# Kernel tuning notes

Hardware: AMD Instinct MI355X
Metric: run time of the kernel (lower is better)

Reference implementation:

```python
import jax, jax.numpy as jnp
import numpy as np

BETA = 20.0  # Softplus beta in the original torch module
# upper-triangular (offset=1) indices of a 3x3 matrix, matching torch.triu_indices(3,3,1)
TRIU_R = np.array([0, 0, 1])
TRIU_C = np.array([1, 2, 2])


def _softplus(x):
    # torch.nn.Softplus(beta=20): log(1+exp(beta*x))/beta, numerically stable via jax.nn.softplus
    return jax.nn.softplus(BETA * x) / BETA


def setup_inputs() -> dict:
    key = jax.random.key(0)
    ks = jax.random.split(key, 9)
    N = 1_000_000
    h = 32

    def lin_init(k, fan_in, fan_out):
        bound = 1.0 / np.sqrt(fan_in)
        kw, kb = jax.random.split(k)
        W = jax.random.uniform(kw, (fan_in, fan_out), jnp.float32, -bound, bound)
        b = jax.random.uniform(kb, (fan_out,), jnp.float32, -bound, bound)
        return W, b

    x = jax.random.normal(ks[0], (N, 3), jnp.float32)
    W1, b1 = lin_init(ks[1], 3, h)
    W2, b2 = lin_init(ks[2], h, h)
    W3, b3 = lin_init(ks[3], h, h)
    W4, b4 = lin_init(ks[4], h, 3)
    return {"x": x, "W1": W1, "b1": b1, "W2": W2, "b2": b2,
            "W3": W3, "b3": b3, "W4": W4, "b4": b4}


def reference(x, W1, b1, W2, b2, W3, b3, W4, b4):
    def mlp(p):  # p: [3] -> [3] (the 3 free entries of the antisymmetric matrix)
        h = _softplus(p @ W1 + b1)
        h = _softplus(h @ W2 + b2)
        h = _softplus(h @ W3 + b3)
        return h @ W4 + b4

    def pres_A(p):  # p: [3] -> antisymmetric [3,3]
        v = mlp(p)
        M = jnp.zeros((3, 3), dtype=p.dtype).at[TRIU_R, TRIU_C].set(v)
        return M - M.T

    # per-sample Jacobian dA/dx: [N, 3, 3, 3]
    J = jax.vmap(jax.jacrev(pres_A))(x.reshape(-1, 3))
    # trace over (column, x-dim): out[n, a] = sum_i dA[n, a, i]/dx[n, i]
    return jnp.einsum('naii->na', J)
```

## Files before the change

kernel.cpp:

```cpp
#include <hip/hip_runtime.h>
#include <math.h>

#define NTHR 256
#define WAVES_PER_BLOCK 4

typedef __attribute__((ext_vector_type(8))) _Float16 f16x8;
typedef __attribute__((ext_vector_type(2))) _Float16 half2v;
typedef __attribute__((ext_vector_type(4))) float f32x4;
typedef __attribute__((ext_vector_type(4))) unsigned uint4v;

#define CEXP 28.85390082f
#define KLOG 0.03465735903f

#define EXP2F(v) __builtin_amdgcn_exp2f(v)
#define LOG2F(v) __builtin_amdgcn_logf(v)

static __device__ __forceinline__ float act_hs(float z, float& s) {
    float cz = CEXP * z;
    float e  = EXP2F(-fabsf(cz));
    float p  = 1.0f + e;
    float r  = __builtin_amdgcn_rcpf(p);
    s = (z >= 0.0f) ? r : (1.0f - r);
    return fmaxf(z, 0.0f) + KLOG * LOG2F(p);
}
static __device__ __forceinline__ float sigmoid20(float z) {
    float e = EXP2F(-CEXP * z);
    return __builtin_amdgcn_rcpf(1.0f + e);
}

static __device__ __forceinline__ unsigned pk(float a, float b) {
    return __builtin_bit_cast(unsigned, __builtin_amdgcn_cvt_pkrtz(a, b));
}

static __device__ __forceinline__ f16x8 pack8(const float* v) {
    uint4v u = {pk(v[0], v[1]), pk(v[2], v[3]), pk(v[4], v[5]), pk(v[6], v[7])};
    return __builtin_bit_cast(f16x8, u);
}
static __device__ __forceinline__ void fsplit8(const float* v, f16x8& hi, f16x8& lo) {
    unsigned h[4], l[4];
    #pragma unroll
    for (int p = 0; p < 4; ++p) {
        float a = v[2 * p], b = v[2 * p + 1];
        unsigned hp = pk(a, b);
        half2v hh = __builtin_bit_cast(half2v, hp);
        h[p] = hp;
        l[p] = pk(a - (float)hh[0], b - (float)hh[1]);
    }
    hi = __builtin_bit_cast(f16x8, (uint4v){h[0], h[1], h[2], h[3]});
    lo = __builtin_bit_cast(f16x8, (uint4v){l[0], l[1], l[2], l[3]});
}

static __device__ __forceinline__ void fsplit_cc(const f32x4& c0, const f32x4& c1,
                                                 f16x8& hi, f16x8& lo) {
    float v[8] = {c0[0], c0[1], c0[2], c0[3], c1[0], c1[1], c1[2], c1[3]};
    fsplit8(v, hi, lo);
}
static __device__ __forceinline__ f16x8 pack_cc(const f32x4& c0, const f32x4& c1) {
    uint4v u = {pk(c0[0], c0[1]), pk(c0[2], c0[3]), pk(c1[0], c1[1]), pk(c1[2], c1[3])};
    return __builtin_bit_cast(f16x8, u);
}

static __device__ __forceinline__ f32x4 mfma3(f16x8 wh, f16x8 wl, f16x8 bh, f16x8 bl, f32x4 c) {
    c = __builtin_amdgcn_mfma_f32_16x16x32_f16(wh, bh, c, 0, 0, 0);
    c = __builtin_amdgcn_mfma_f32_16x16x32_f16(wh, bl, c, 0, 0, 0);
    c = __builtin_amdgcn_mfma_f32_16x16x32_f16(wl, bh, c, 0, 0, 0);
    return c;
}
static __device__ __forceinline__ f32x4 mfma2(f16x8 wh, f16x8 wl, f16x8 b, f32x4 c) {
    c = __builtin_amdgcn_mfma_f32_16x16x32_f16(wh, b, c, 0, 0, 0);
    c = __builtin_amdgcn_mfma_f32_16x16x32_f16(wl, b, c, 0, 0, 0);
    return c;
}

static __device__ __forceinline__ void split1h(float v, _Float16& hi, _Float16& lo) {
    _Float16 h = (_Float16)v;
    hi = h;
    lo = (_Float16)(v - (float)h);
}

__global__ void __launch_bounds__(NTHR)
presdiv_kernel(const float* __restrict__ x,
               const float* __restrict__ W1, const float* __restrict__ b1,
               const float* __restrict__ W2, const float* __restrict__ b2,
               const float* __restrict__ W3, const float* __restrict__ b3,
               const float* __restrict__ W4,
               float* __restrict__ out, int N)
{
    const int lane = threadIdx.x & 63;
    const int wid  = threadIdx.x >> 6;
    const int n16  = lane & 15;
    const int g    = lane >> 4;

    f16x8 w2h[2], w2l[2], w3h[2], w3l[2];
    #pragma unroll
    for (int h = 0; h < 2; ++h) {
        #pragma unroll
        for (int j = 0; j < 8; ++j) {
            _Float16 hi, lo;
            const int k2 = g * 8 + j;
            split1h(W2[k2 * 32 + 16 * h + n16], hi, lo);
            w2h[h][j] = hi; w2l[h][j] = lo;
            const int k3 = (j < 4) ? (4 * g + j) : (16 + 4 * g + (j - 4));
            split1h(W3[k3 * 32 + 16 * h + n16], hi, lo);
            w3h[h][j] = hi; w3l[h][j] = lo;
        }
    }
    float w1r[3][8], bb1[8];
    #pragma unroll
    for (int j = 0; j < 8; ++j) {
        bb1[j] = b1[g * 8 + j];
        #pragma unroll
        for (int d = 0; d < 3; ++d) w1r[d][j] = W1[d * 32 + g * 8 + j];
    }
    float bb2[2][4], bb3[2][4], w4r[2][4][3];
    #pragma unroll
    for (int h = 0; h < 2; ++h)
        #pragma unroll
        for (int r = 0; r < 4; ++r) {
            const int row = 16 * h + 4 * g + r;
            bb2[h][r] = b2[row];
            bb3[h][r] = b3[row];
            #pragma unroll
            for (int k = 0; k < 3; ++k) w4r[h][r][k] = W4[row * 3 + k];
        }

    const int ntiles = (N + 15) >> 4;
    const int nwaves = gridDim.x * WAVES_PER_BLOCK;
    const f32x4 vzero = {0.f, 0.f, 0.f, 0.f};

    for (int tile = blockIdx.x * WAVES_PER_BLOCK + wid; tile < ntiles; tile += nwaves) {
        int s = tile * 16 + n16;
        if (s >= N) s = N - 1;
        const float x0 = x[3 * s + 0];
        const float x1 = x[3 * s + 1];
        const float x2 = x[3 * s + 2];

        float vF[8], v0[8], v1[8], v2[8];
        #pragma unroll
        for (int j = 0; j < 8; ++j) {
            float z = bb1[j];
            z = fmaf(x0, w1r[0][j], z);
            z = fmaf(x1, w1r[1][j], z);
            z = fmaf(x2, w1r[2][j], z);
            float sg; vF[j] = act_hs(z, sg);
            v0[j] = sg * w1r[0][j];
            v1[j] = sg * w1r[1][j];
            v2[j] = sg * w1r[2][j];
        }

        f32x4 aF[2], a0[2], a1[2], a2[2];
        aF[0] = (f32x4){bb2[0][0], bb2[0][1], bb2[0][2], bb2[0][3]};
        aF[1] = (f32x4){bb2[1][0], bb2[1][1], bb2[1][2], bb2[1][3]};
        a0[0] = a0[1] = a1[0] = a1[1] = a2[0] = a2[1] = vzero;

        f16x8 bh, bl;
        fsplit8(vF, bh, bl);
        aF[0] = mfma3(w2h[0], w2l[0], bh, bl, aF[0]);
        aF[1] = mfma3(w2h[1], w2l[1], bh, bl, aF[1]);
        f16x8 tb = pack8(v0);
        a0[0] = mfma2(w2h[0], w2l[0], tb, a0[0]);
        a0[1] = mfma2(w2h[1], w2l[1], tb, a0[1]);
        tb = pack8(v1);
        a1[0] = mfma2(w2h[0], w2l[0], tb, a1[0]);
        a1[1] = mfma2(w2h[1], w2l[1], tb, a1[1]);
        tb = pack8(v2);
        a2[0] = mfma2(w2h[0], w2l[0], tb, a2[0]);
        a2[1] = mfma2(w2h[1], w2l[1], tb, a2[1]);

        #pragma unroll
        for (int h = 0; h < 2; ++h)
            #pragma unroll
            for (int r = 0; r < 4; ++r) {
                float s2v;
                aF[h][r] = act_hs(aF[h][r], s2v);
                a0[h][r] *= s2v;
                a1[h][r] *= s2v;
                a2[h][r] *= s2v;
            }

        f32x4 zF[2], u0[2], u1[2], u2[2];
        zF[0] = (f32x4){bb3[0][0], bb3[0][1], bb3[0][2], bb3[0][3]};
        zF[1] = (f32x4){bb3[1][0], bb3[1][1], bb3[1][2], bb3[1][3]};
        u0[0] = u0[1] = u1[0] = u1[1] = u2[0] = u2[1] = vzero;

        fsplit_cc(aF[0], aF[1], bh, bl);
        zF[0] = mfma3(w3h[0], w3l[0], bh, bl, zF[0]);
        zF[1] = mfma3(w3h[1], w3l[1], bh, bl, zF[1]);
        tb = pack_cc(a0[0], a0[1]);
        u0[0] = mfma2(w3h[0], w3l[0], tb, u0[0]);
        u0[1] = mfma2(w3h[1], w3l[1], tb, u0[1]);
        tb = pack_cc(a1[0], a1[1]);
        u1[0] = mfma2(w3h[0], w3l[0], tb, u1[0]);
        u1[1] = mfma2(w3h[1], w3l[1], tb, u1[1]);
        tb = pack_cc(a2[0], a2[1]);
        u2[0] = mfma2(w3h[0], w3l[0], tb, u2[0]);
        u2[1] = mfma2(w3h[1], w3l[1], tb, u2[1]);

        float o0 = 0.f, o1 = 0.f, o2 = 0.f;
        #pragma unroll
        for (int h = 0; h < 2; ++h)
            #pragma unroll
            for (int r = 0; r < 4; ++r) {
                const float s3v = sigmoid20(zF[h][r]);
                const float t0v = s3v * u0[h][r];
                const float t1v = s3v * u1[h][r];
                const float t2v = s3v * u2[h][r];
                const float w0 = w4r[h][r][0], w1 = w4r[h][r][1], w2 = w4r[h][r][2];
                o0 = fmaf(t1v, w0, fmaf(t2v, w1, o0));
                o1 = fmaf(-t0v, w0, fmaf(t2v, w2, o1));
                o2 = fmaf(-t0v, w1, fmaf(-t1v, w2, o2));
            }

        o0 += __shfl_xor(o0, 16); o0 += __shfl_xor(o0, 32);
        o1 += __shfl_xor(o1, 16); o1 += __shfl_xor(o1, 32);
        o2 += __shfl_xor(o2, 16); o2 += __shfl_xor(o2, 32);

        if (g == 0) {
            out[3 * s + 0] = o0;
            out[3 * s + 1] = o1;
            out[3 * s + 2] = o2;
        }
    }
}

extern "C" void kernel_launch(void* const* d_in, const int* in_sizes, int n_in,
                              void* d_out, int out_size, void* d_ws, size_t ws_size,
                              hipStream_t stream)
{
    const float* x  = (const float*)d_in[0];
    const float* W1 = (const float*)d_in[1];
    const float* b1 = (const float*)d_in[2];
    const float* W2 = (const float*)d_in[3];
    const float* b2 = (const float*)d_in[4];
    const float* W3 = (const float*)d_in[5];
    const float* b3 = (const float*)d_in[6];
    const float* W4 = (const float*)d_in[7];
    float* out = (float*)d_out;

    const int N = in_sizes[0] / 3;
    const int blocks = 4096;
    presdiv_kernel<<<blocks, NTHR, 0, stream>>>(x, W1, b1, W2, b2, W3, b3, W4, out, N);
}
```

Before: 154.0 us.

## Cut register pressure by reloading biases per tile and target five blocks per CU

Biases b1/b2/b3 and W4 are no longer held in registers for the whole kernel. They are re-read inside the tile loop with volatile vector loads. Launch bounds now request 5 blocks per SIMD/CU, and the grid shrinks to 1280 persistent blocks, aiming for higher occupancy. The softplus/sigmoid helper is rewritten to use exp2 and log2 instead of rcp, trading one op for another. The cost is extra per-tile memory/cache loads that volatile prevents the compiler from hoisting.

```diff
diff --git a/kernel.cpp b/kernel.cpp
--- a/kernel.cpp
+++ b/kernel.cpp
@@ -3,6 +3,7 @@
 
 #define NTHR 256
 #define WAVES_PER_BLOCK 4
+#define NBLOCKS 1280
 
 typedef __attribute__((ext_vector_type(8))) _Float16 f16x8;
 typedef __attribute__((ext_vector_type(2))) _Float16 half2v;
@@ -18,14 +19,18 @@
 static __device__ __forceinline__ float act_hs(float z, float& s) {
     float cz = CEXP * z;
     float e  = EXP2F(-fabsf(cz));
-    float p  = 1.0f + e;
-    float r  = __builtin_amdgcn_rcpf(p);
-    s = (z >= 0.0f) ? r : (1.0f - r);
-    return fmaxf(z, 0.0f) + KLOG * LOG2F(p);
+    float l  = LOG2F(1.0f + e);
+    float zp = fmaxf(z, 0.0f);
+    s = 1.0f - EXP2F(fmaf(-CEXP, zp, -l));
+    return fmaf(KLOG, l, zp);
 }
 static __device__ __forceinline__ float sigmoid20(float z) {
     float e = EXP2F(-CEXP * z);
     return __builtin_amdgcn_rcpf(1.0f + e);
+}
+
+static __device__ __forceinline__ f32x4 vload4(const float* p) {
+    return *(const volatile f32x4*)p;
 }
 
 static __device__ __forceinline__ unsigned pk(float a, float b) {
@@ -78,7 +83,7 @@
     lo = (_Float16)(v - (float)h);
 }
 
-__global__ void __launch_bounds__(NTHR)
+__global__ void __launch_bounds__(NTHR, 5)
 presdiv_kernel(const float* __restrict__ x,
                const float* __restrict__ W1, const float* __restrict__ b1,
                const float* __restrict__ W2, const float* __restrict__ b2,
@@ -105,27 +110,15 @@
             w3h[h][j] = hi; w3l[h][j] = lo;
         }
     }
-    float w1r[3][8], bb1[8];
+    float w1r[3][8];
     #pragma unroll
     for (int j = 0; j < 8; ++j) {
-        bb1[j] = b1[g * 8 + j];
         #pragma unroll
         for (int d = 0; d < 3; ++d) w1r[d][j] = W1[d * 32 + g * 8 + j];
     }
-    float bb2[2][4], bb3[2][4], w4r[2][4][3];
-    #pragma unroll
-    for (int h = 0; h < 2; ++h)
-        #pragma unroll
-        for (int r = 0; r < 4; ++r) {
-            const int row = 16 * h + 4 * g + r;
-            bb2[h][r] = b2[row];
-            bb3[h][r] = b3[row];
-            #pragma unroll
-            for (int k = 0; k < 3; ++k) w4r[h][r][k] = W4[row * 3 + k];
-        }
 
     const int ntiles = (N + 15) >> 4;
-    const int nwaves = gridDim.x * WAVES_PER_BLOCK;
+    const int nwaves = NBLOCKS * WAVES_PER_BLOCK;
     const f32x4 vzero = {0.f, 0.f, 0.f, 0.f};
 
     for (int tile = blockIdx.x * WAVES_PER_BLOCK + wid; tile < ntiles; tile += nwaves) {
@@ -135,10 +128,13 @@
         const float x1 = x[3 * s + 1];
         const float x2 = x[3 * s + 2];
 
+        const f32x4 b1a = vload4(b1 + 8 * g);
+        const f32x4 b1b = vload4(b1 + 8 * g + 4);
+
         float vF[8], v0[8], v1[8], v2[8];
         #pragma unroll
         for (int j = 0; j < 8; ++j) {
-            float z = bb1[j];
+            float z = (j < 4) ? b1a[j & 3] : b1b[j & 3];
             z = fmaf(x0, w1r[0][j], z);
             z = fmaf(x1, w1r[1][j], z);
             z = fmaf(x2, w1r[2][j], z);
@@ -149,8 +145,8 @@
         }
 
         f32x4 aF[2], a0[2], a1[2], a2[2];
-        aF[0] = (f32x4){bb2[0][0], bb2[0][1], bb2[0][2], bb2[0][3]};
-        aF[1] = (f32x4){bb2[1][0], bb2[1][1], bb2[1][2], bb2[1][3]};
+        aF[0] = vload4(b2 + 4 * g);
+        aF[1] = vload4(b2 + 16 + 4 * g);
         a0[0] = a0[1] = a1[0] = a1[1] = a2[0] = a2[1] = vzero;
 
         f16x8 bh, bl;
@@ -179,8 +175,8 @@
             }
 
         f32x4 zF[2], u0[2], u1[2], u2[2];
-        zF[0] = (f32x4){bb3[0][0], bb3[0][1], bb3[0][2], bb3[0][3]};
-        zF[1] = (f32x4){bb3[1][0], bb3[1][1], bb3[1][2], bb3[1][3]};
+        zF[0] = vload4(b3 + 4 * g);
+        zF[1] = vload4(b3 + 16 + 4 * g);
         u0[0] = u0[1] = u1[0] = u1[1] = u2[0] = u2[1] = vzero;
 
         fsplit_cc(aF[0], aF[1], bh, bl);
@@ -198,18 +194,26 @@
 
         float o0 = 0.f, o1 = 0.f, o2 = 0.f;
         #pragma unroll
-        for (int h = 0; h < 2; ++h)
+        for (int h = 0; h < 2; ++h) {
+            const int base = (16 * h + 4 * g) * 3;
+            const f32x4 wa = vload4(W4 + base);
+            const f32x4 wb = vload4(W4 + base + 4);
+            const f32x4 wc = vload4(W4 + base + 8);
+            const float wf[12] = {wa[0], wa[1], wa[2], wa[3],
+                                  wb[0], wb[1], wb[2], wb[3],
+                                  wc[0], wc[1], wc[2], wc[3]};
             #pragma unroll
             for (int r = 0; r < 4; ++r) {
                 const float s3v = sigmoid20(zF[h][r]);
                 const float t0v = s3v * u0[h][r];
                 const float t1v = s3v * u1[h][r];
                 const float t2v = s3v * u2[h][r];
-                const float w0 = w4r[h][r][0], w1 = w4r[h][r][1], w2 = w4r[h][r][2];
+                const float w0 = wf[3 * r], w1 = wf[3 * r + 1], w2 = wf[3 * r + 2];
                 o0 = fmaf(t1v, w0, fmaf(t2v, w1, o0));
                 o1 = fmaf(-t0v, w0, fmaf(t2v, w2, o1));
                 o2 = fmaf(-t0v, w1, fmaf(-t1v, w2, o2));
             }
+        }
 
         o0 += __shfl_xor(o0, 16); o0 += __shfl_xor(o0, 32);
         o1 += __shfl_xor(o1, 16); o1 += __shfl_xor(o1, 32);
@@ -238,6 +242,5 @@
     float* out = (float*)d_out;
 
     const int N = in_sizes[0] / 3;
-    const int blocks = 4096;
-    presdiv_kernel<<<blocks, NTHR, 0, stream>>>(x, W1, b1, W2, b2, W3, b3, W4, out, N);
-}
+    presdiv_kernel<<<NBLOCKS, NTHR, 0, stream>>>(x, W1, b1, W2, b2, W3, b3, W4, out, N);
+}
```

Result: slower. 194.6 us (+26.4%).
